# Kernel optimization log

Measured on AMD Instinct MI355X. Metric: run time of the kernel, lower is better.

Reference implementation:

```python
import jax, jax.numpy as jnp
import numpy as np

B, H, W, DIM, HEADS, WS = 32, 56, 56, 192, 6, 7
KD = DIM // HEADS          # key_dim = head_dim = 32 (attn_ratio=1.0 -> d = KD, dh = DIM)
DH = KD * HEADS
HQKV = DH + 2 * KD * HEADS # 576
L = H * W
HIDDEN = 4 * DIM
NWIN = (H // WS) * (W // WS)
NTOK = WS * WS
SCALE = KD ** -0.5


def _bias_idxs(ws):
    pts = [(i, j) for i in range(ws) for j in range(ws)]
    offs, idxs = {}, []
    for p1 in pts:
        for p2 in pts:
            o = (abs(p1[0] - p2[0]), abs(p1[1] - p2[1]))
            if o not in offs:
                offs[o] = len(offs)
            idxs.append(offs[o])
    return np.asarray(idxs, np.int32).reshape(ws * ws, ws * ws), len(offs)

BIAS_IDX, NOFF = _bias_idxs(WS)  # [49,49], 49 distinct offsets


def _ln(x, g, b, eps=1e-5):
    m = x.mean(-1, keepdims=True)
    v = jnp.mean((x - m) ** 2, -1, keepdims=True)
    return (x - m) * jax.lax.rsqrt(v + eps) * g + b


def setup_inputs() -> dict:
    key = jax.random.key(0)
    ks = jax.random.split(key, 8)
    f32 = jnp.float32
    return {
        "x": jax.random.normal(ks[0], (B, L, DIM), f32),
        "ln1_g": jnp.ones((DIM,), f32), "ln1_b": jnp.zeros((DIM,), f32),
        "qkv_w": jax.random.normal(ks[1], (DIM, HQKV), f32) * 0.02,
        "qkv_b": jnp.zeros((HQKV,), f32),
        "proj_w": jax.random.normal(ks[2], (DH, DIM), f32) * 0.02,
        "proj_b": jnp.zeros((DIM,), f32),
        "attn_bias": jax.random.normal(ks[3], (HEADS, NOFF), f32) * 0.02,
        "conv_w": jax.random.normal(ks[4], (DIM, 1, 3, 3), f32) * 0.1,  # depthwise OIHW
        "bn_g": jnp.ones((DIM,), f32), "bn_b": jnp.zeros((DIM,), f32),
        "bn_m": jnp.zeros((DIM,), f32), "bn_v": jnp.ones((DIM,), f32),
        "ln2_g": jnp.ones((DIM,), f32), "ln2_b": jnp.zeros((DIM,), f32),
        "fc1_w": jax.random.normal(ks[5], (DIM, HIDDEN), f32) * 0.02,
        "fc1_b": jnp.zeros((HIDDEN,), f32),
        "fc2_w": jax.random.normal(ks[6], (HIDDEN, DIM), f32) * 0.02,
        "fc2_b": jnp.zeros((DIM,), f32),
    }


def reference(x, ln1_g, ln1_b, qkv_w, qkv_b, proj_w, proj_b, attn_bias,
              conv_w, bn_g, bn_b, bn_m, bn_v, ln2_g, ln2_b,
              fc1_w, fc1_b, fc2_w, fc2_b):
    # ---- window partition: [B,L,C] -> [B*nWin, 49, C] (H,W divisible by WS, no pad)
    xw = x.reshape(B, H // WS, WS, W // WS, WS, DIM)
    xw = xw.transpose(0, 1, 3, 2, 4, 5).reshape(B * NWIN, NTOK, DIM)
    # ---- attention (pre-LN inside Attention module)
    h = _ln(xw, ln1_g, ln1_b)
    qkv = (h @ qkv_w + qkv_b).reshape(B * NWIN, NTOK, HEADS, 3 * KD)
    qkv = qkv.transpose(0, 2, 1, 3)                      # [Bw, heads, N, 3*KD]
    q, k, v = qkv[..., :KD], qkv[..., KD:2 * KD], qkv[..., 2 * KD:]
    bias = attn_bias[:, BIAS_IDX]                        # [heads, 49, 49] gathered table
    scores = jnp.einsum('bhnd,bhmd->bhnm', q, k) * SCALE + bias[None]
    a = jax.nn.softmax(scores, axis=-1)
    o = jnp.einsum('bhnm,bhmd->bhnd', a, v)
    o = o.transpose(0, 2, 1, 3).reshape(B * NWIN, NTOK, DH)
    o = o @ proj_w + proj_b
    # ---- window unpartition -> [B,L,C], residual add
    o = o.reshape(B, H // WS, W // WS, WS, WS, DIM)
    o = o.transpose(0, 1, 3, 2, 4, 5).reshape(B, L, DIM)
    x = x + o
    # ---- depthwise 3x3 conv + BN (eval-mode) in NCHW
    xc = x.transpose(0, 2, 1).reshape(B, DIM, H, W)
    xc = jax.lax.conv_general_dilated(
        xc, conv_w, window_strides=(1, 1), padding=[(1, 1), (1, 1)],
        feature_group_count=DIM, dimension_numbers=('NCHW', 'OIHW', 'NCHW'))
    inv = jax.lax.rsqrt(bn_v + 1e-5)
    xc = (xc - bn_m[None, :, None, None]) * (inv * bn_g)[None, :, None, None] + bn_b[None, :, None, None]
    x = xc.reshape(B, DIM, L).transpose(0, 2, 1)
    # ---- MLP (LN -> fc1 -> GELU(exact) -> fc2) with residual
    h2 = _ln(x, ln2_g, ln2_b)
    h2 = jax.nn.gelu(h2 @ fc1_w + fc1_b, approximate=False)
    h2 = h2 @ fc2_w + fc2_b
    return x + h2
```

## Files before the change

### kernel.cpp

```cpp
#include <hip/hip_runtime.h>
#include <hip/hip_bf16.h>

#define DIMC 192
#define LTOT 3136

using bf16x8 = __attribute__((ext_vector_type(8))) short;
using f32x4  = __attribute__((ext_vector_type(4))) float;

static __device__ __forceinline__ unsigned short f2bf(float f) {
  unsigned u = __builtin_bit_cast(unsigned, f);
  u = (u + 0x7FFFu + ((u >> 16) & 1u)) >> 16;
  return (unsigned short)u;
}
static __device__ __forceinline__ float bf2f(unsigned short u) {
  unsigned v = ((unsigned)u) << 16;
  return __builtin_bit_cast(float, v);
}
static __device__ __forceinline__ int iabs(int a) { return a < 0 ? -a : a; }

static __device__ __forceinline__ void gload16(const unsigned short* g, unsigned short* lds) {
  __builtin_amdgcn_global_load_lds(
      (const __attribute__((address_space(1))) void*)g,
      (__attribute__((address_space(3))) void*)lds, 16, 0, 0);
}

__global__ __launch_bounds__(256) void prep_k(
    const float* __restrict__ qkv_w, const float* __restrict__ proj_w,
    const float* __restrict__ fc1_w, const float* __restrict__ fc2_w,
    const float* __restrict__ conv_w,
    const float* __restrict__ bn_g, const float* __restrict__ bn_b,
    const float* __restrict__ bn_m, const float* __restrict__ bn_v,
    unsigned short* __restrict__ qkvT, unsigned short* __restrict__ projT,
    unsigned short* __restrict__ fc1T, unsigned short* __restrict__ fc2T,
    float* __restrict__ convT, float* __restrict__ bnsc, float* __restrict__ bnsh)
{
  int idx = blockIdx.x * 256 + threadIdx.x;
  if (idx < 122880) { int n = idx / 192, k = idx % 192;
    qkvT[idx] = (n < 576) ? f2bf(qkv_w[k * 576 + n]) : 0; return; }
  idx -= 122880;
  if (idx < 49152)  { int n = idx / 192, k = idx % 192;
    projT[idx] = (n < 192) ? f2bf(proj_w[k * 192 + n]) : 0; return; }
  idx -= 49152;
  if (idx < 147456) { int n = idx / 192, k = idx % 192;
    fc1T[idx] = f2bf(fc1_w[k * 768 + n]); return; }
  idx -= 147456;
  if (idx < 196608) { int n = idx / 768, k = idx % 768;
    fc2T[idx] = (n < 192) ? f2bf(fc2_w[k * 192 + n]) : 0; return; }
  idx -= 196608;
  if (idx < 1728)   { int tap = idx / 192, c = idx % 192; convT[idx] = conv_w[c * 9 + tap]; return; }
  idx -= 1728;
  if (idx < 192) {
    float s = bn_g[idx] * rsqrtf(bn_v[idx] + 1e-5f);
    bnsc[idx] = s; bnsh[idx] = bn_b[idx] - bn_m[idx] * s;
  }
}

__global__ __launch_bounds__(256) void qkvg_k(
    const float* __restrict__ x, const float* __restrict__ ln_g, const float* __restrict__ ln_b,
    const unsigned short* __restrict__ qkvT,
    const float* __restrict__ qkv_b, unsigned short* __restrict__ qkv)
{
  __shared__ unsigned short LB[12288];
  const int tid = threadIdx.x;
  const int l = tid & 63, wv = tid >> 6;
  const int u = l >> 4, ll = l & 15;
  const int m0 = blockIdx.x * 64;

  {
    const int row = tid >> 2, part = tid & 3;
    const int m = m0 + row;
    const int w = m / 49, t = m % 49;
    const int bb = w >> 6, win = w & 63;
    const int lpix = ((win >> 3) * 7 + t / 7) * 56 + (win & 7) * 7 + t % 7;
    const float* rowp = x + ((size_t)bb * LTOT + lpix) * DIMC + part * 48;
    float4 v[12];
    float s = 0.f, ss = 0.f;
    #pragma unroll
    for (int i = 0; i < 12; ++i) {
      v[i] = *(const float4*)(rowp + i * 4);
      s  += v[i].x + v[i].y + v[i].z + v[i].w;
      ss += v[i].x * v[i].x + v[i].y * v[i].y + v[i].z * v[i].z + v[i].w * v[i].w;
    }
    s += __shfl_xor(s, 1); ss += __shfl_xor(ss, 1);
    s += __shfl_xor(s, 2); ss += __shfl_xor(ss, 2);
    float mean = s * (1.f / 192.f);
    float rstd = rsqrtf(ss * (1.f / 192.f) - mean * mean + 1e-5f);
    const float* gp = ln_g + part * 48;
    const float* bp = ln_b + part * 48;
    #pragma unroll
    for (int i = 0; i < 12; ++i) {
      float4 gg = *(const float4*)(gp + i * 4);
      float4 bb4 = *(const float4*)(bp + i * 4);
      ushort4 o;
      o.x = f2bf((v[i].x - mean) * rstd * gg.x + bb4.x);
      o.y = f2bf((v[i].y - mean) * rstd * gg.y + bb4.y);
      o.z = f2bf((v[i].z - mean) * rstd * gg.z + bb4.z);
      o.w = f2bf((v[i].w - mean) * rstd * gg.w + bb4.w);
      int cbyte = part * 96 + i * 8;
      *(ushort4*)((char*)LB + row * 384 + (cbyte ^ ((row & 7) << 4))) = o;
    }
  }
  __syncthreads();

  bf16x8 areg[6];
  #pragma unroll
  for (int kk = 0; kk < 6; ++kk) {
    int cb = (kk * 64 + u * 16) ^ ((ll & 7) << 4);
    areg[kk] = *(const bf16x8*)((const char*)LB + (wv * 16 + ll) * 384 + cb);
  }

  for (int c = 0; c < 9; ++c) {
    __syncthreads();
    const char* Wg = (const char*)(qkvT + (size_t)c * 64 * 192);
    #pragma unroll
    for (int i = 0; i < 6; ++i) {
      int ob = i * 4096 + tid * 16;
      int r = ob / 384, cc = ob % 384;
      int cs = cc ^ ((r & 7) << 4);
      gload16((const unsigned short*)(Wg + r * 384 + cs), &LB[ob >> 1]);
    }
    __syncthreads();
    f32x4 p1[4] = {};
    #pragma unroll
    for (int kk = 0; kk < 6; ++kk) {
      int cb = (kk * 64 + u * 16) ^ ((ll & 7) << 4);
      #pragma unroll
      for (int nf = 0; nf < 4; ++nf) {
        bf16x8 bfr = *(const bf16x8*)((const char*)LB + (nf * 16 + ll) * 384 + cb);
        p1[nf] = __builtin_amdgcn_mfma_f32_16x16x32_bf16(areg[kk], bfr, p1[nf], 0, 0, 0);
      }
    }
    #pragma unroll
    for (int nf = 0; nf < 4; ++nf)
    #pragma unroll
    for (int r = 0; r < 4; ++r) {
      int m = m0 + wv * 16 + u * 4 + r;
      int n = c * 64 + nf * 16 + ll;
      qkv[(size_t)m * 576 + n] = f2bf(p1[nf][r] + qkv_b[n]);
    }
  }
}

__global__ __launch_bounds__(256) void attnp_k(
    const unsigned short* __restrict__ qkv, const float* __restrict__ attn_bias,
    const unsigned short* __restrict__ projT, const float* __restrict__ proj_b,
    const float* __restrict__ x, unsigned short* __restrict__ x1b)
{
  __shared__ unsigned short Qs[2560];
  __shared__ unsigned short Ks[2560];
  __shared__ unsigned short Vt[2304];
  __shared__ unsigned short Ps[4608];
  __shared__ float bias_s[52];
  const int tid = threadIdx.x;
  const int l = tid & 63, wv = tid >> 6;
  const int u = l >> 4, ll = l & 15;
  const int w = blockIdx.x, b = w >> 6, win = w & 63;
  const f32x4 fz = {0.f, 0.f, 0.f, 0.f};

  for (int i = tid; i < 15 * 40; i += 256) {
    Qs[(49 + i / 40) * 40 + i % 40] = 0;
    Ks[(49 + i / 40) * 40 + i % 40] = 0;
  }
  for (int i = tid; i < 32 * 15; i += 256) Vt[(i / 15) * 72 + 49 + i % 15] = 0;

  f32x4 pacc[4][3] = {};

  for (int h = 0; h < 6; ++h) {
    __syncthreads();
    if (tid < 49) bias_s[tid] = attn_bias[h * 49 + tid];
    #pragma unroll
    for (int it = 0; it < 3; ++it) {
      int idx = tid + it * 256;
      if (idx < 588) {
        int row = idx / 12, g = idx % 12;
        int4 v = *(const int4*)&qkv[((size_t)w * 49 + row) * 576 + h * 96 + g * 8];
        if (g < 4) *(int4*)&Qs[row * 40 + g * 8] = v;
        else if (g < 8) *(int4*)&Ks[row * 40 + (g - 4) * 8] = v;
        else {
          union { int4 v4; unsigned short us[8]; } uu; uu.v4 = v;
          int d0 = (g - 8) * 8;
          #pragma unroll
          for (int e = 0; e < 8; ++e) Vt[(d0 + e) * 72 + row] = uu.us[e];
        }
      }
    }
    __syncthreads();

    {
      const int qr = wv * 16 + ll;
      const int qi = qr > 48 ? 48 : qr;
      bf16x8 qf = *(const bf16x8*)&Qs[(wv * 16 + ll) * 40 + u * 8];
      f32x4 sc[4];
      #pragma unroll
      for (int kt = 0; kt < 4; ++kt) {
        bf16x8 kf = *(const bf16x8*)&Ks[(kt * 16 + ll) * 40 + u * 8];
        sc[kt] = __builtin_amdgcn_mfma_f32_16x16x32_bf16(kf, qf, fz, 0, 0, 0);
      }
      float sv[4][4];
      float mx = -1e30f;
      #pragma unroll
      for (int kt = 0; kt < 4; ++kt)
        #pragma unroll
        for (int r = 0; r < 4; ++r) {
          int kr = kt * 16 + u * 4 + r;
          float val = -1e30f;
          if (kr < 49)
            val = sc[kt][r] * 0.17677669529663689f +
                  bias_s[iabs(qi / 7 - kr / 7) * 7 + iabs(qi % 7 - kr % 7)];
          sv[kt][r] = val;
          mx = fmaxf(mx, val);
        }
      mx = fmaxf(mx, __shfl_xor(mx, 16));
      mx = fmaxf(mx, __shfl_xor(mx, 32));
      float sum = 0.f;
      #pragma unroll
      for (int kt = 0; kt < 4; ++kt)
        #pragma unroll
        for (int r = 0; r < 4; ++r) {
          float p = __expf(sv[kt][r] - mx);
          sv[kt][r] = p; sum += p;
        }
      sum += __shfl_xor(sum, 16);
      sum += __shfl_xor(sum, 32);
      float inv = 1.f / sum;
      #pragma unroll
      for (int kt = 0; kt < 4; ++kt)
        #pragma unroll
        for (int r = 0; r < 4; ++r)
          Ps[(wv * 16 + ll) * 72 + kt * 16 + u * 4 + r] = f2bf(sv[kt][r] * inv);
    }
    __syncthreads();

    {
      f32x4 oa[2] = {fz, fz};
      #pragma unroll
      for (int kk = 0; kk < 2; ++kk) {
        bf16x8 pf = *(const bf16x8*)&Ps[(wv * 16 + ll) * 72 + kk * 32 + u * 8];
        #pragma unroll
        for (int nt = 0; nt < 2; ++nt) {
          bf16x8 vf = *(const bf16x8*)&Vt[(nt * 16 + ll) * 72 + kk * 32 + u * 8];
          oa[nt] = __builtin_amdgcn_mfma_f32_16x16x32_bf16(pf, vf, oa[nt], 0, 0, 0);
        }
      }
      #pragma unroll
      for (int nt = 0; nt < 2; ++nt)
        #pragma unroll
        for (int r = 0; r < 4; ++r)
          Qs[(wv * 16 + u * 4 + r) * 40 + nt * 16 + ll] = f2bf(oa[nt][r]);
    }
    __syncthreads();

    {
      bf16x8 af[4], bfr[3];
      #pragma unroll
      for (int mt = 0; mt < 4; ++mt)
        af[mt] = *(const bf16x8*)&Qs[(mt * 16 + ll) * 40 + u * 8];
      #pragma unroll
      for (int nf = 0; nf < 3; ++nf)
        bfr[nf] = *(const bf16x8*)&projT[(size_t)(wv * 48 + nf * 16 + ll) * 192 + h * 32 + u * 8];
      #pragma unroll
      for (int mt = 0; mt < 4; ++mt)
        #pragma unroll
        for (int nf = 0; nf < 3; ++nf)
          pacc[mt][nf] = __builtin_amdgcn_mfma_f32_16x16x32_bf16(af[mt], bfr[nf], pacc[mt][nf], 0, 0, 0);
    }
  }

  #pragma unroll
  for (int mt = 0; mt < 4; ++mt)
  #pragma unroll
  for (int r = 0; r < 4; ++r) {
    int m = mt * 16 + u * 4 + r;
    if (m < 49) {
      int lpix = ((win >> 3) * 7 + m / 7) * 56 + (win & 7) * 7 + m % 7;
      size_t base = ((size_t)b * LTOT + lpix) * DIMC;
      #pragma unroll
      for (int nf = 0; nf < 3; ++nf) {
        int n = wv * 48 + nf * 16 + ll;
        float val = pacc[mt][nf][r] + proj_b[n] + x[base + n];
        x1b[base + n] = f2bf(val);
      }
    }
  }
}

__global__ __launch_bounds__(256) void fmlp_k(
    const unsigned short* __restrict__ h2, const unsigned short* __restrict__ fc1T,
    const float* __restrict__ fc1_b, const unsigned short* __restrict__ fc2T,
    const float* __restrict__ fc2_b, const unsigned short* __restrict__ x2,
    float* __restrict__ out)
{
  __shared__ unsigned short W1[6144];
  __shared__ unsigned short W2[6144];
  __shared__ unsigned short P[2048];
  const int tid = threadIdx.x;
  const int l = tid & 63, wv = tid >> 6;
  const int u = l >> 4, ll = l & 15;
  const int m0 = blockIdx.x * 64;
  f32x4 acc[12] = {};

  bf16x8 areg[6];
  {
    const unsigned short* arow = h2 + (size_t)(m0 + wv * 16 + ll) * 192;
    #pragma unroll
    for (int kk = 0; kk < 6; ++kk)
      areg[kk] = *(const bf16x8*)(arow + kk * 32 + u * 8);
  }

  for (int c = 0; c < 24; ++c) {
    if (c) __syncthreads();
    const char* W1g = (const char*)(fc1T + (size_t)c * 32 * 192);
    #pragma unroll
    for (int i = 0; i < 3; ++i) {
      int ob = i * 4096 + tid * 16;
      int r = ob / 384, cc = ob % 384;
      int cs = cc ^ ((r & 7) << 4);
      gload16((const unsigned short*)(W1g + r * 384 + cs), &W1[ob >> 1]);
    }
    #pragma unroll
    for (int i = 0; i < 3; ++i) {
      int unit = i * 256 + tid;
      int r = unit >> 2, q = unit & 3;
      int4 vv = *(const int4*)&fc2T[(size_t)r * 768 + c * 32 + q * 8];
      *(int4*)((char*)W2 + r * 64 + ((q * 16) ^ (((r >> 1) & 3) << 4))) = vv;
    }
    __syncthreads();

    {
      f32x4 p1[2] = {};
      #pragma unroll
      for (int kk = 0; kk < 6; ++kk) {
        int cb = (kk * 64 + u * 16) ^ ((ll & 7) << 4);
        #pragma unroll
        for (int nf = 0; nf < 2; ++nf) {
          bf16x8 bfr = *(const bf16x8*)((const char*)W1 + (nf * 16 + ll) * 384 + cb);
          p1[nf] = __builtin_amdgcn_mfma_f32_16x16x32_bf16(areg[kk], bfr, p1[nf], 0, 0, 0);
        }
      }
      #pragma unroll
      for (int nf = 0; nf < 2; ++nf)
      #pragma unroll
      for (int r = 0; r < 4; ++r) {
        int mrow = wv * 16 + u * 4 + r;
        int n = nf * 16 + ll;
        float v = p1[nf][r] + fc1_b[c * 32 + n];
        float gl = v / (1.f + __expf(-1.702f * v));
        *(unsigned short*)((char*)P + mrow * 64 + ((n * 2) ^ (((mrow >> 1) & 3) << 4))) = f2bf(gl);
      }
    }
    {
      bf16x8 af2 = *(const bf16x8*)((const char*)P + (wv * 16 + ll) * 64 +
                                    ((u * 16) ^ (((ll >> 1) & 3) << 4)));
      #pragma unroll
      for (int nt = 0; nt < 12; ++nt) {
        bf16x8 bfr = *(const bf16x8*)((const char*)W2 + (nt * 16 + ll) * 64 +
                                      ((u * 16) ^ (((ll >> 1) & 3) << 4)));
        acc[nt] = __builtin_amdgcn_mfma_f32_16x16x32_bf16(af2, bfr, acc[nt], 0, 0, 0);
      }
    }
  }
  #pragma unroll
  for (int nt = 0; nt < 12; ++nt)
  #pragma unroll
  for (int r = 0; r < 4; ++r) {
    int m = m0 + wv * 16 + u * 4 + r;
    int n = nt * 16 + ll;
    size_t o = (size_t)m * 192 + n;
    out[o] = acc[nt][r] + fc2_b[n] + bf2f(x2[o]);
  }
}

__global__ __launch_bounds__(256) void conv_k(
    const unsigned short* __restrict__ x1b, const float* __restrict__ wT,
    const float* __restrict__ bnsc, const float* __restrict__ bnsh,
    const float* __restrict__ g2, const float* __restrict__ b2,
    unsigned short* __restrict__ x2, unsigned short* __restrict__ h2)
{
  const int bid = blockIdx.x;
  const int swz = (bid & 7) * 784 + (bid >> 3);
  const int grp = threadIdx.x >> 6, l = threadIdx.x & 63;
  const int qq = swz * 4 + grp;
  const int b = qq / 784, rem = qq % 784;
  const int pix0 = rem * 4;
  const int i = pix0 / 56, j = pix0 % 56;
  const bool act = l < 48;
  const int c = l * 4;
  float4 a[4];
  #pragma unroll
  for (int p = 0; p < 4; ++p) a[p] = make_float4(0.f, 0.f, 0.f, 0.f);
  if (act) {
    #pragma unroll
    for (int di = -1; di <= 1; ++di) {
      int ni = i + di;
      if (ni < 0 || ni >= 56) continue;
      #pragma unroll
      for (int djx = 0; djx < 6; ++djx) {
        int nj = j - 1 + djx;
        float4 vv = make_float4(0.f, 0.f, 0.f, 0.f);
        if (nj >= 0 && nj < 56) {
          ushort4 sv = *(const ushort4*)&x1b[((size_t)b * LTOT + ni * 56 + nj) * DIMC + c];
          vv.x = bf2f(sv.x); vv.y = bf2f(sv.y); vv.z = bf2f(sv.z); vv.w = bf2f(sv.w);
        }
        #pragma unroll
        for (int p = 0; p < 4; ++p) {
          int dj = djx - p;
          if (dj >= 0 && dj <= 2) {
            float4 w = *(const float4*)&wT[((di + 1) * 3 + dj) * DIMC + c];
            a[p].x += vv.x * w.x; a[p].y += vv.y * w.y;
            a[p].z += vv.z * w.z; a[p].w += vv.w * w.w;
          }
        }
      }
    }
    float4 s4 = *(const float4*)&bnsc[c];
    float4 h4 = *(const float4*)&bnsh[c];
    #pragma unroll
    for (int p = 0; p < 4; ++p) {
      a[p].x = a[p].x * s4.x + h4.x; a[p].y = a[p].y * s4.y + h4.y;
      a[p].z = a[p].z * s4.z + h4.z; a[p].w = a[p].w * s4.w + h4.w;
      ushort4 xv;
      xv.x = f2bf(a[p].x); xv.y = f2bf(a[p].y); xv.z = f2bf(a[p].z); xv.w = f2bf(a[p].w);
      *(ushort4*)&x2[((size_t)b * LTOT + i * 56 + j + p) * DIMC + c] = xv;
    }
  }
  #pragma unroll
  for (int p = 0; p < 4; ++p) {
    float s = act ? a[p].x + a[p].y + a[p].z + a[p].w : 0.f;
    float ss = act ? a[p].x * a[p].x + a[p].y * a[p].y + a[p].z * a[p].z + a[p].w * a[p].w : 0.f;
    #pragma unroll
    for (int off = 1; off < 64; off <<= 1) { s += __shfl_xor(s, off); ss += __shfl_xor(ss, off); }
    float mean = s * (1.f / 192.f);
    float rstd = rsqrtf(ss * (1.f / 192.f) - mean * mean + 1e-5f);
    if (act) {
      float4 gg = *(const float4*)&g2[c];
      float4 bb = *(const float4*)&b2[c];
      ushort4 ov;
      ov.x = f2bf((a[p].x - mean) * rstd * gg.x + bb.x);
      ov.y = f2bf((a[p].y - mean) * rstd * gg.y + bb.y);
      ov.z = f2bf((a[p].z - mean) * rstd * gg.z + bb.z);
      ov.w = f2bf((a[p].w - mean) * rstd * gg.w + bb.w);
      *(ushort4*)&h2[((size_t)b * LTOT + i * 56 + j + p) * DIMC + c] = ov;
    }
  }
}

extern "C" void kernel_launch(void* const* d_in, const int* in_sizes, int n_in,
                              void* d_out, int out_size, void* d_ws, size_t ws_size,
                              hipStream_t stream) {
  const float* x      = (const float*)d_in[0];
  const float* ln1_g  = (const float*)d_in[1];
  const float* ln1_b  = (const float*)d_in[2];
  const float* qkv_w  = (const float*)d_in[3];
  const float* qkv_b  = (const float*)d_in[4];
  const float* proj_w = (const float*)d_in[5];
  const float* proj_b = (const float*)d_in[6];
  const float* attn_b = (const float*)d_in[7];
  const float* conv_w = (const float*)d_in[8];
  const float* bn_g   = (const float*)d_in[9];
  const float* bn_b   = (const float*)d_in[10];
  const float* bn_m   = (const float*)d_in[11];
  const float* bn_v   = (const float*)d_in[12];
  const float* ln2_g  = (const float*)d_in[13];
  const float* ln2_b  = (const float*)d_in[14];
  const float* fc1_w  = (const float*)d_in[15];
  const float* fc1_b  = (const float*)d_in[16];
  const float* fc2_w  = (const float*)d_in[17];
  const float* fc2_b  = (const float*)d_in[18];
  float* out = (float*)d_out;

  const size_t AOFF = 1048576, BOFF = AOFF + 115605504;
  const size_t NEEDED = BOFF + 38535168;
  if (ws_size < NEEDED) return;

  char* ws = (char*)d_ws;
  unsigned short* qkvT  = (unsigned short*)(ws);
  unsigned short* projT = (unsigned short*)(ws + 245760);
  unsigned short* fc1T  = (unsigned short*)(ws + 344064);
  unsigned short* fc2T  = (unsigned short*)(ws + 638976);
  float*          convT = (float*)(ws + 1032192);
  float*          bnsc  = (float*)(ws + 1039104);
  float*          bnsh  = (float*)(ws + 1039872);

  unsigned short* qkv = (unsigned short*)(ws + AOFF);
  unsigned short* x2  = (unsigned short*)(ws + AOFF);
  unsigned short* h2  = (unsigned short*)(ws + AOFF + 38535168);
  unsigned short* x1b = (unsigned short*)(ws + BOFF);

  prep_k<<<2024, 256, 0, stream>>>(qkv_w, proj_w, fc1_w, fc2_w, conv_w,
                                   bn_g, bn_b, bn_m, bn_v,
                                   qkvT, projT, fc1T, fc2T, convT, bnsc, bnsh);
  qkvg_k<<<1568, 256, 0, stream>>>(x, ln1_g, ln1_b, qkvT, qkv_b, qkv);
  attnp_k<<<2048, 256, 0, stream>>>(qkv, attn_b, projT, proj_b, x, x1b);
  conv_k<<<6272, 256, 0, stream>>>(x1b, convT, bnsc, bnsh, ln2_g, ln2_b, x2, h2);
  fmlp_k<<<1568, 256, 0, stream>>>(h2, fc1T, fc1_b, fc2T, fc2_b, x2, out);
}
```

Measured before the change: 330.7 us.

## Double-buffer fc1 weights and register-prefetch fc2 weights in fused MLP kernel

Adds a second LDS buffer for the fc1 weight chunk and issues asynchronous global-to-LDS loads for the next chunk while the current chunk is computed. fc2 weight chunks are prefetched into registers and written to LDS after the compute, between two barriers. The aim is to hide global load latency behind MFMA work in the 24-step hidden loop. In exchange it uses more LDS, more registers and one extra barrier per step, which could lower occupancy.

```diff
diff --git a/kernel.cpp b/kernel.cpp
--- a/kernel.cpp
+++ b/kernel.cpp
@@ -290,7 +290,7 @@
     const float* __restrict__ fc2_b, const unsigned short* __restrict__ x2,
     float* __restrict__ out)
 {
-  __shared__ unsigned short W1[6144];
+  __shared__ unsigned short W1[2][6144];
   __shared__ unsigned short W2[6144];
   __shared__ unsigned short P[2048];
   const int tid = threadIdx.x;
@@ -307,24 +307,47 @@
       areg[kk] = *(const bf16x8*)(arow + kk * 32 + u * 8);
   }
 
-  for (int c = 0; c < 24; ++c) {
-    if (c) __syncthreads();
-    const char* W1g = (const char*)(fc1T + (size_t)c * 32 * 192);
+  {
+    const char* W1g = (const char*)(fc1T);
     #pragma unroll
     for (int i = 0; i < 3; ++i) {
       int ob = i * 4096 + tid * 16;
       int r = ob / 384, cc = ob % 384;
       int cs = cc ^ ((r & 7) << 4);
-      gload16((const unsigned short*)(W1g + r * 384 + cs), &W1[ob >> 1]);
+      gload16((const unsigned short*)(W1g + r * 384 + cs), &W1[0][ob >> 1]);
     }
     #pragma unroll
     for (int i = 0; i < 3; ++i) {
       int unit = i * 256 + tid;
       int r = unit >> 2, q = unit & 3;
-      int4 vv = *(const int4*)&fc2T[(size_t)r * 768 + c * 32 + q * 8];
+      int4 vv = *(const int4*)&fc2T[(size_t)r * 768 + q * 8];
       *(int4*)((char*)W2 + r * 64 + ((q * 16) ^ (((r >> 1) & 3) << 4))) = vv;
     }
-    __syncthreads();
+  }
+  __syncthreads();
+
+  for (int c = 0; c < 24; ++c) {
+    const int cur = c & 1;
+    int4 w2r0, w2r1, w2r2;
+    if (c < 23) {
+      const char* W1g = (const char*)(fc1T + (size_t)(c + 1) * 32 * 192);
+      #pragma unroll
+      for (int i = 0; i < 3; ++i) {
+        int ob = i * 4096 + tid * 16;
+        int r = ob / 384, cc = ob % 384;
+        int cs = cc ^ ((r & 7) << 4);
+        gload16((const unsigned short*)(W1g + r * 384 + cs), &W1[cur ^ 1][ob >> 1]);
+      }
+      {
+        int unit = tid;
+        int r = unit >> 2, q = unit & 3;
+        w2r0 = *(const int4*)&fc2T[(size_t)r * 768 + (c + 1) * 32 + q * 8];
+        unit = 256 + tid; r = unit >> 2; q = unit & 3;
+        w2r1 = *(const int4*)&fc2T[(size_t)r * 768 + (c + 1) * 32 + q * 8];
+        unit = 512 + tid; r = unit >> 2; q = unit & 3;
+        w2r2 = *(const int4*)&fc2T[(size_t)r * 768 + (c + 1) * 32 + q * 8];
+      }
+    }
 
     {
       f32x4 p1[2] = {};
@@ -333,7 +356,7 @@
         int cb = (kk * 64 + u * 16) ^ ((ll & 7) << 4);
         #pragma unroll
         for (int nf = 0; nf < 2; ++nf) {
-          bf16x8 bfr = *(const bf16x8*)((const char*)W1 + (nf * 16 + ll) * 384 + cb);
+          bf16x8 bfr = *(const bf16x8*)((const char*)W1[cur] + (nf * 16 + ll) * 384 + cb);
           p1[nf] = __builtin_amdgcn_mfma_f32_16x16x32_bf16(areg[kk], bfr, p1[nf], 0, 0, 0);
         }
       }
@@ -358,6 +381,17 @@
         acc[nt] = __builtin_amdgcn_mfma_f32_16x16x32_bf16(af2, bfr, acc[nt], 0, 0, 0);
       }
     }
+    __syncthreads();
+    if (c < 23) {
+      int unit = tid;
+      int r = unit >> 2, q = unit & 3;
+      *(int4*)((char*)W2 + r * 64 + ((q * 16) ^ (((r >> 1) & 3) << 4))) = w2r0;
+      unit = 256 + tid; r = unit >> 2; q = unit & 3;
+      *(int4*)((char*)W2 + r * 64 + ((q * 16) ^ (((r >> 1) & 3) << 4))) = w2r1;
+      unit = 512 + tid; r = unit >> 2; q = unit & 3;
+      *(int4*)((char*)W2 + r * 64 + ((q * 16) ^ (((r >> 1) & 3) << 4))) = w2r2;
+    }
+    __syncthreads();
   }
   #pragma unroll
   for (int nt = 0; nt < 12; ++nt)
```

New measurement: 333.8 us. About the same (+0.9%).
